# Kernel optimization log

Measured on AMD Instinct MI355X. Metric: run time of the kernel, lower is better.

The kernel has to match this reference:

```python
import jax, jax.numpy as jnp
import numpy as np

DIM, HEADS, HEAD_DIM = 1024, 16, 64
B, L, S = 4, 2048, 2048
EPS = 1e-5
NEG_INF = -1e9


def rms_norm(x, w):
    # x: [..., d]; normalize over last dim, scale by learned weight w [d]
    var = jnp.mean(jnp.square(x), axis=-1, keepdims=True)
    return x * jax.lax.rsqrt(var + EPS) * w


def setup_inputs() -> dict:
    key = jax.random.key(0)
    ks = jax.random.split(key, 9)
    hd = HEADS * HEAD_DIM
    scale = 1.0 / np.sqrt(DIM)
    return {
        "q": jax.random.normal(ks[0], (B, L, DIM), dtype=jnp.float32),
        "kv": jax.random.normal(ks[1], (B, S, DIM), dtype=jnp.float32),
        "x_seqlens": jax.random.randint(ks[2], (B,), 1, S + 1, dtype=jnp.int32),
        "Wq": jax.random.normal(ks[3], (DIM, hd), dtype=jnp.float32) * scale,
        "Wk": jax.random.normal(ks[4], (DIM, hd), dtype=jnp.float32) * scale,
        "Wv": jax.random.normal(ks[5], (DIM, hd), dtype=jnp.float32) * scale,
        "Wo": jax.random.normal(ks[6], (hd, DIM), dtype=jnp.float32) * (1.0 / np.sqrt(hd)),
        "q_norm_w": jnp.ones((HEAD_DIM,), dtype=jnp.float32),
        "k_norm_w": jnp.ones((HEAD_DIM,), dtype=jnp.float32),
    }


def reference(q, kv, x_seqlens, Wq, Wk, Wv, Wo, q_norm_w, k_norm_w):
    b, l, _ = q.shape
    s = kv.shape[1]
    # QKV projections -> [b, h, n, d]
    qh = (q @ Wq).reshape(b, l, HEADS, HEAD_DIM).transpose(0, 2, 1, 3)
    kh = (kv @ Wk).reshape(b, s, HEADS, HEAD_DIM).transpose(0, 2, 1, 3)
    vh = (kv @ Wv).reshape(b, s, HEADS, HEAD_DIM).transpose(0, 2, 1, 3)
    # per-head RMSNorm on q and k
    qh = rms_norm(qh, q_norm_w)
    kh = rms_norm(kh, k_norm_w)
    # dense padding mask [b, 1, 1, s]: True where kv position is valid
    mask = (jnp.arange(s, dtype=jnp.int32)[None, :] < x_seqlens[:, None])[:, None, None, :]
    # scaled dot-product attention (math path: full score matrix)
    scores = jnp.einsum("bhld,bhsd->bhls", qh, kh) * (1.0 / np.sqrt(HEAD_DIM))
    scores = jnp.where(mask, scores, NEG_INF)
    attn = jax.nn.softmax(scores, axis=-1)
    o = jnp.einsum("bhls,bhsd->bhld", attn, vh)  # [b, h, l, d]
    o = o.transpose(0, 2, 1, 3).reshape(b, l, HEADS * HEAD_DIM)
    return o @ Wo
```

## Files before the change

### kernel.cpp

```cpp
#include <hip/hip_runtime.h>
#include <hip/hip_bf16.h>
#include <stdint.h>

#define BB 4
#define LL 2048
#define SS 2048
#define DIMM 1024
#define HH 16
#define HD 64
#define NHD 1024

typedef __bf16 bf16_t;
typedef __bf16 bf16x8 __attribute__((ext_vector_type(8)));
typedef __bf16 bf16x4 __attribute__((ext_vector_type(4)));
typedef float f32x4 __attribute__((ext_vector_type(4)));

#define GLDS16(g, l) __builtin_amdgcn_global_load_lds( \
    (const __attribute__((address_space(1))) void*)(g), \
    (__attribute__((address_space(3))) void*)(l), 16, 0, 0)

#define FENCED_BARRIER() do {                    \
    asm volatile("" ::: "memory");               \
    __builtin_amdgcn_s_barrier();                \
    asm volatile("" ::: "memory");               \
    __builtin_amdgcn_sched_barrier(0);           \
  } while (0)

#define SWZ(o) ((o) ^ ((((o) >> 7) & 7) << 4))

__global__ __launch_bounds__(256) void cvt_all(const float* __restrict__ q,
                                               const float* __restrict__ kv,
                                               bf16_t* __restrict__ Aq,
                                               bf16_t* __restrict__ Akv) {
  const int bi = blockIdx.x;
  const float* in = (bi < 4096) ? q : kv;
  bf16_t* out = (bi < 4096) ? Aq : Akv;
  size_t i = ((size_t)(bi & 4095) * 256 + threadIdx.x) * 8;
  const f32x4* p = (const f32x4*)(in + i);
  f32x4 a = p[0], b = p[1];
  bf16x8 o;
#pragma unroll
  for (int j = 0; j < 4; ++j) { o[j] = (bf16_t)a[j]; o[4 + j] = (bf16_t)b[j]; }
  *(bf16x8*)(out + i) = o;
}

__global__ __launch_bounds__(256) void transpose_all(
    const float* __restrict__ W0, const float* __restrict__ W1,
    const float* __restrict__ W2, const float* __restrict__ W3,
    bf16_t* __restrict__ O0, bf16_t* __restrict__ O1,
    bf16_t* __restrict__ O2, bf16_t* __restrict__ O3) {
  const float* in = (blockIdx.z == 0) ? W0 : (blockIdx.z == 1) ? W1
                    : (blockIdx.z == 2) ? W2 : W3;
  bf16_t* out = (blockIdx.z == 0) ? O0 : (blockIdx.z == 1) ? O1
                : (blockIdx.z == 2) ? O2 : O3;
  __shared__ float tile[64][65];
  const int r0 = blockIdx.y * 64, c0 = blockIdx.x * 64;
  const int tr = threadIdx.x >> 2;
  const int tc4 = (threadIdx.x & 3) * 16;
#pragma unroll
  for (int i = 0; i < 4; ++i) {
    f32x4 v = *(const f32x4*)&in[(size_t)(r0 + tr) * 1024 + c0 + tc4 + i * 4];
    tile[tr][tc4 + i * 4 + 0] = v.x;
    tile[tr][tc4 + i * 4 + 1] = v.y;
    tile[tr][tc4 + i * 4 + 2] = v.z;
    tile[tr][tc4 + i * 4 + 3] = v.w;
  }
  __syncthreads();
#pragma unroll
  for (int i = 0; i < 2; ++i) {
    bf16x8 o;
#pragma unroll
    for (int j = 0; j < 8; ++j) o[j] = (bf16_t)tile[tc4 + i * 8 + j][tr];
    *(bf16x8*)&out[(size_t)(c0 + tr) * 1024 + r0 + tc4 + i * 8] = o;
  }
}

__global__ __launch_bounds__(512, 1) void proj_qkv(
    const bf16_t* __restrict__ Aq, const bf16_t* __restrict__ Akv,
    const bf16_t* __restrict__ WqT, const bf16_t* __restrict__ WkT,
    const bf16_t* __restrict__ WvT,
    bf16_t* __restrict__ Qb, bf16_t* __restrict__ Kb, bf16_t* __restrict__ Vt,
    const float* __restrict__ qw, const float* __restrict__ kw, float qscale) {
  __shared__ bf16_t Lds[2][3][8192];
  const int nt = blockIdx.x;
  const int mode = nt >> 3;
  const bf16_t* A  = (mode == 0) ? Aq : Akv;
  const bf16_t* Bt = (mode == 0) ? WqT : (mode == 1 ? WkT : WvT);
  const int n0 = (nt & 7) * 128;
  const int m0 = blockIdx.y * 256;
  const int tid = threadIdx.x, lane = tid & 63, w = tid >> 6;
  const int wr = w >> 1, wc = w & 1;
  const int fr = lane & 15, fg = lane >> 4;
  f32x4 acc[4][4] = {};

  auto stageKT = [&](int kt, int d) {
#pragma unroll
    for (int ht = 0; ht < 3; ++ht) {
#pragma unroll
      for (int c = 0; c < 2; ++c) {
        const int o = (c * 512 + tid) * 16;
        const int eff = SWZ(o);
        const int rl = eff >> 7, ce = (eff & 127) >> 1;
        const bf16_t* src = (ht < 2)
            ? A  + (size_t)(m0 + ht * 128 + rl) * 1024 + kt * 64 + ce
            : Bt + (size_t)(n0 + rl) * 1024 + kt * 64 + ce;
        GLDS16(src, &Lds[d][ht][c * 4096 + w * 512]);
      }
    }
  };

  stageKT(0, 0);
  int cur = 0;
  for (int kt = 0; kt < 16; ++kt) {
    if (kt + 1 < 16) {
      stageKT(kt + 1, cur ^ 1);
      asm volatile("s_waitcnt vmcnt(6)" ::: "memory");
    } else {
      asm volatile("s_waitcnt vmcnt(0)" ::: "memory");
    }
    FENCED_BARRIER();

    bf16x8 af[4][2], bf[4][2];
#pragma unroll
    for (int m = 0; m < 4; ++m)
#pragma unroll
      for (int ks = 0; ks < 2; ++ks) {
        const int row = wr * 64 + m * 16 + fr;
        const int o = (row & 127) * 128 + ks * 64 + fg * 16;
        af[m][ks] = *(const bf16x8*)&Lds[cur][row >> 7][SWZ(o) >> 1];
      }
#pragma unroll
    for (int n = 0; n < 4; ++n)
#pragma unroll
      for (int ks = 0; ks < 2; ++ks) {
        const int row = wc * 64 + n * 16 + fr;
        const int o = row * 128 + ks * 64 + fg * 16;
        bf[n][ks] = *(const bf16x8*)&Lds[cur][2][SWZ(o) >> 1];
      }
    __builtin_amdgcn_s_setprio(1);
#pragma unroll
    for (int m = 0; m < 4; ++m)
#pragma unroll
      for (int n = 0; n < 4; ++n)
#pragma unroll
        for (int ks = 0; ks < 2; ++ks)
          acc[m][n] = __builtin_amdgcn_mfma_f32_16x16x32_bf16(
              af[m][ks], bf[n][ks], acc[m][n], 0, 0, 0);
    __builtin_amdgcn_s_setprio(0);
    FENCED_BARRIER();
    cur ^= 1;
  }

  if (mode <= 1) {
    const float* nw = (mode == 0) ? qw : kw;
    const float ps = (mode == 0) ? qscale : 1.0f;
    bf16_t* Cb = (mode == 0) ? Qb : Kb;
    float w4[4];
#pragma unroll
    for (int n = 0; n < 4; ++n) w4[n] = nw[n * 16 + fr] * ps;
#pragma unroll
    for (int m = 0; m < 4; ++m) {
      float ss[4];
#pragma unroll
      for (int j = 0; j < 4; ++j) {
        ss[j] = 0.f;
#pragma unroll
        for (int n = 0; n < 4; ++n) ss[j] += acc[m][n][j] * acc[m][n][j];
      }
#pragma unroll
      for (int d = 1; d < 16; d <<= 1)
#pragma unroll
        for (int j = 0; j < 4; ++j) ss[j] += __shfl_xor(ss[j], d);
      float rs[4];
#pragma unroll
      for (int j = 0; j < 4; ++j) rs[j] = rsqrtf(ss[j] * (1.f / 64.f) + 1e-5f);
#pragma unroll
      for (int n = 0; n < 4; ++n)
#pragma unroll
        for (int j = 0; j < 4; ++j) {
          size_t row = (size_t)m0 + wr * 64 + m * 16 + fg * 4 + j;
          size_t col = (size_t)n0 + wc * 64 + n * 16 + fr;
          Cb[row * NHD + col] = (bf16_t)(acc[m][n][j] * rs[j] * w4[n]);
        }
    }
  } else {
#pragma unroll
    for (int m = 0; m < 4; ++m) {
      int r = m0 + wr * 64 + m * 16 + fg * 4;
      int bb_ = r >> 11, s0 = r & 2047;
#pragma unroll
      for (int n = 0; n < 4; ++n) {
        int cc = n0 + wc * 64 + n * 16 + fr;
        int hh_ = cc >> 6, dd = cc & 63;
        bf16x4 pk;
#pragma unroll
        for (int j = 0; j < 4; ++j) pk[j] = (bf16_t)acc[m][n][j];
        *(bf16x4*)&Vt[(((size_t)bb_ * 16 + hh_) * 64 + dd) * 2048 + s0] = pk;
      }
    }
  }
}

__global__ __launch_bounds__(256) void gemm_out(const bf16_t* __restrict__ A,
                                                const bf16_t* __restrict__ Bt,
                                                float* __restrict__ Cout) {
  __shared__ bf16_t As[2][4096];
  __shared__ bf16_t Bs[2][4096];
  const int K = 1024, N = 1024;
  const int tid = threadIdx.x, lane = tid & 63, w = tid >> 6;
  const int m0 = blockIdx.y * 128, n0 = blockIdx.x * 128;
  const int wm = (w >> 1) * 64, wn = (w & 1) * 64;
  const int fr = lane & 15, fg = lane >> 4;
  f32x4 acc[4][4] = {};

  auto stage = [&](int kt, int bi) {
    const int kb = kt * 32;
#pragma unroll
    for (int j = 0; j < 2; ++j) {
      int e = (j * 4 + w) * 512 + lane * 8;
      int r = e >> 5, c = e & 31;
      GLDS16(A  + (size_t)(m0 + r) * K + kb + c, &As[bi][(j * 4 + w) * 512]);
      GLDS16(Bt + (size_t)(n0 + r) * K + kb + c, &Bs[bi][(j * 4 + w) * 512]);
    }
  };

  stage(0, 0);
  int cur = 0;
  for (int kt = 0; kt < 32; ++kt) {
    if (kt + 1 < 32) {
      stage(kt + 1, cur ^ 1);
      asm volatile("s_waitcnt vmcnt(4)" ::: "memory");
    } else {
      asm volatile("s_waitcnt vmcnt(0)" ::: "memory");
    }
    FENCED_BARRIER();
    bf16x8 a[4], b[4];
#pragma unroll
    for (int m = 0; m < 4; ++m) a[m] = *(const bf16x8*)&As[cur][(wm + m * 16 + fr) * 32 + fg * 8];
#pragma unroll
    for (int n = 0; n < 4; ++n) b[n] = *(const bf16x8*)&Bs[cur][(wn + n * 16 + fr) * 32 + fg * 8];
    __builtin_amdgcn_s_setprio(1);
#pragma unroll
    for (int m = 0; m < 4; ++m)
#pragma unroll
      for (int n = 0; n < 4; ++n)
        acc[m][n] = __builtin_amdgcn_mfma_f32_16x16x32_bf16(a[m], b[n], acc[m][n], 0, 0, 0);
    __builtin_amdgcn_s_setprio(0);
    FENCED_BARRIER();
    cur ^= 1;
  }
#pragma unroll
  for (int m = 0; m < 4; ++m)
#pragma unroll
    for (int n = 0; n < 4; ++n)
#pragma unroll
      for (int j = 0; j < 4; ++j) {
        size_t row = (size_t)m0 + wm + m * 16 + fg * 4 + j;
        size_t col = (size_t)n0 + wn + n * 16 + fr;
        Cout[row * N + col] = acc[m][n][j];
      }
}

__global__ __launch_bounds__(256, 3) void attn64(const bf16_t* __restrict__ Qb,
                                                 const bf16_t* __restrict__ Kb,
                                                 const bf16_t* __restrict__ Vtg,
                                                 bf16_t* __restrict__ Ob,
                                                 const int* __restrict__ seqlens) {
  __shared__ bf16_t Kl[2][4096];
  __shared__ bf16_t Vl[2][4096];
  __shared__ bf16_t Pl[8192];
  const int tid = threadIdx.x, lane = tid & 63, w = tid >> 6;
  const int fr = lane & 15, fg = lane >> 4;
  const int qt = blockIdx.x, bh = blockIdx.y;
  const int b = bh >> 4, h = bh & 15;
  const int seqlen = seqlens[b];
  const int ntiles = (seqlen + 63) >> 6;
  bf16_t* Pw = &Pl[w * 2048];

  const bf16_t* qp = Qb + ((size_t)b * LL + qt * 128 + w * 32 + fr) * NHD + h * 64;
  bf16x8 qf[2][2];
#pragma unroll
  for (int qs = 0; qs < 2; ++qs) {
    qf[qs][0] = *(const bf16x8*)&qp[(size_t)qs * 16 * NHD + fg * 8];
    qf[qs][1] = *(const bf16x8*)&qp[(size_t)qs * 16 * NHD + 32 + fg * 8];
  }
  asm volatile("s_waitcnt vmcnt(0)" ::: "memory");

  const bf16_t* Kg = Kb + (size_t)b * SS * NHD + h * 64;
  const bf16_t* Vg = Vtg + ((size_t)(b * 16 + h)) * 64 * SS;

  auto stage = [&](int t, int bi) {
#pragma unroll
    for (int c = 0; c < 2; ++c) {
      const int ro = (w * 2 + c) * 8 + (lane >> 3);
      const int cs = ((lane & 7) ^ (ro & 7)) * 8;
      GLDS16(Kg + (size_t)(t * 64 + ro) * NHD + cs, &Kl[bi][(w * 2 + c) * 512]);
      GLDS16(Vg + (size_t)ro * SS + t * 64 + cs, &Vl[bi][(w * 2 + c) * 512]);
    }
  };

  bf16x8 vones;
#pragma unroll
  for (int i = 0; i < 8; ++i) vones[i] = (bf16_t)1.0f;

  f32x4 oacc[2][4] = {};
  f32x4 lacc[2] = {};
  const float M0 = 12.0f;

  auto softmax_strip = [&](f32x4 (&s)[4], int qs, int t) {
    if (t == ntiles - 1 && (seqlen & 63)) {
#pragma unroll
      for (int n = 0; n < 4; ++n) {
        bool valid = (t * 64 + n * 16 + fr) < seqlen;
#pragma unroll
        for (int j = 0; j < 4; ++j) s[n][j] = valid ? s[n][j] : -1e30f;
      }
    }
#pragma unroll
    for (int n = 0; n < 4; ++n)
#pragma unroll
      for (int j = 0; j < 4; ++j) s[n][j] = __builtin_exp2f(s[n][j] - M0);
#pragma unroll
    for (int n = 0; n < 4; ++n)
#pragma unroll
      for (int j = 0; j < 4; ++j) {
        const int prow = qs * 16 + fg * 4 + j;
        const int pcol = n * 16 + fr;
        Pw[prow * 64 + (((pcol >> 3) ^ (prow & 7)) * 8) + (pcol & 7)] =
            (bf16_t)s[n][j];
      }
  };

  stage(0, 0);
  int cur = 0;
  for (int t = 0; t < ntiles; ++t) {
    if (t + 1 < ntiles) {
      stage(t + 1, cur ^ 1);
      asm volatile("s_waitcnt vmcnt(4)" ::: "memory");
    } else {
      asm volatile("s_waitcnt vmcnt(0)" ::: "memory");
    }
    FENCED_BARRIER();

    f32x4 s0[4] = {}, s1[4] = {};
    __builtin_amdgcn_s_setprio(1);
#pragma unroll
    for (int n = 0; n < 4; ++n) {
      const int rr = n * 16 + fr;
      bf16x8 kf0 = *(const bf16x8*)&Kl[cur][rr * 64 + ((fg ^ (rr & 7)) * 8)];
      bf16x8 kf1 = *(const bf16x8*)&Kl[cur][rr * 64 + (((fg + 4) ^ (rr & 7)) * 8)];
      s0[n] = __builtin_amdgcn_mfma_f32_16x16x32_bf16(qf[0][0], kf0, s0[n], 0, 0, 0);
      s0[n] = __builtin_amdgcn_mfma_f32_16x16x32_bf16(qf[0][1], kf1, s0[n], 0, 0, 0);
      s1[n] = __builtin_amdgcn_mfma_f32_16x16x32_bf16(qf[1][0], kf0, s1[n], 0, 0, 0);
      s1[n] = __builtin_amdgcn_mfma_f32_16x16x32_bf16(qf[1][1], kf1, s1[n], 0, 0, 0);
    }
    __builtin_amdgcn_s_setprio(0);

    softmax_strip(s0, 0, t);
    softmax_strip(s1, 1, t);

    asm volatile("s_waitcnt lgkmcnt(0)" ::: "memory");
    __builtin_amdgcn_sched_barrier(0);

    __builtin_amdgcn_s_setprio(1);
#pragma unroll
    for (int ks = 0; ks < 2; ++ks) {
      const int pr0 = fr, pr1 = 16 + fr;
      bf16x8 pa0 = *(const bf16x8*)&Pw[pr0 * 64 + (((ks * 4 + fg) ^ (pr0 & 7)) * 8)];
      bf16x8 pa1 = *(const bf16x8*)&Pw[pr1 * 64 + (((ks * 4 + fg) ^ (pr1 & 7)) * 8)];
#pragma unroll
      for (int n = 0; n < 4; ++n) {
        const int rr = n * 16 + fr;
        bf16x8 vf = *(const bf16x8*)&Vl[cur][rr * 64 + (((ks * 4 + fg) ^ (rr & 7)) * 8)];
        oacc[0][n] = __builtin_amdgcn_mfma_f32_16x16x32_bf16(pa0, vf, oacc[0][n], 0, 0, 0);
        oacc[1][n] = __builtin_amdgcn_mfma_f32_16x16x32_bf16(pa1, vf, oacc[1][n], 0, 0, 0);
      }
      lacc[0] = __builtin_amdgcn_mfma_f32_16x16x32_bf16(pa0, vones, lacc[0], 0, 0, 0);
      lacc[1] = __builtin_amdgcn_mfma_f32_16x16x32_bf16(pa1, vones, lacc[1], 0, 0, 0);
    }
    __builtin_amdgcn_s_setprio(0);
    FENCED_BARRIER();
    cur ^= 1;
  }

#pragma unroll
  for (int qs = 0; qs < 2; ++qs) {
    float inv[4];
#pragma unroll
    for (int j = 0; j < 4; ++j) inv[j] = __builtin_amdgcn_rcpf(lacc[qs][j]);
#pragma unroll
    for (int n = 0; n < 4; ++n)
#pragma unroll
      for (int j = 0; j < 4; ++j) {
        size_t row = (size_t)b * LL + qt * 128 + w * 32 + qs * 16 + fg * 4 + j;
        Ob[row * NHD + h * 64 + n * 16 + fr] = (bf16_t)(oacc[qs][n][j] * inv[j]);
      }
  }
}

extern "C" void kernel_launch(void* const* d_in, const int* in_sizes, int n_in,
                              void* d_out, int out_size, void* d_ws, size_t ws_size,
                              hipStream_t stream) {
  const float* q   = (const float*)d_in[0];
  const float* kv  = (const float*)d_in[1];
  const int* seqlens = (const int*)d_in[2];
  const float* Wq = (const float*)d_in[3];
  const float* Wk = (const float*)d_in[4];
  const float* Wv = (const float*)d_in[5];
  const float* Wo = (const float*)d_in[6];
  const float* qw = (const float*)d_in[7];
  const float* kw = (const float*)d_in[8];

  char* ws = (char*)d_ws;
  const size_t MB = 1 << 20;
  bf16_t* Aq  = (bf16_t*)(ws + 0 * MB);
  bf16_t* Akv = (bf16_t*)(ws + 16 * MB);
  bf16_t* WqT = (bf16_t*)(ws + 32 * MB);
  bf16_t* WkT = (bf16_t*)(ws + 34 * MB);
  bf16_t* WvT = (bf16_t*)(ws + 36 * MB);
  bf16_t* WoT = (bf16_t*)(ws + 38 * MB);
  bf16_t* Qb  = (bf16_t*)(ws + 40 * MB);
  bf16_t* Kb  = (bf16_t*)(ws + 56 * MB);
  bf16_t* Vt  = (bf16_t*)(ws + 72 * MB);

  const float QSCALE = 0.125f * 1.44269504088896f;

  cvt_all<<<8192, 256, 0, stream>>>(q, kv, Aq, Akv);
  dim3 tg(16, 16, 4);
  transpose_all<<<tg, 256, 0, stream>>>(Wq, Wk, Wv, Wo, WqT, WkT, WvT, WoT);
  dim3 pg(24, 32);
  proj_qkv<<<pg, 512, 0, stream>>>(Aq, Akv, WqT, WkT, WvT, Qb, Kb, Vt,
                                   qw, kw, QSCALE);
  dim3 ag(LL / 128, BB * HH);
  attn64<<<ag, 256, 0, stream>>>(Qb, Kb, Vt, Aq, seqlens);
  dim3 og(8, 64);
  gemm_out<<<og, 256, 0, stream>>>(Aq, WoT, (float*)d_out);
}
```

Baseline: 187.6 us.

## Shrink QKV projection tiles to 128x128 and give output GEMM K=64 swizzled staging

```diff
diff --git a/kernel.cpp b/kernel.cpp
--- a/kernel.cpp
+++ b/kernel.cpp
@@ -75,36 +75,36 @@
   }
 }
 
-__global__ __launch_bounds__(512, 1) void proj_qkv(
+__global__ __launch_bounds__(256, 2) void proj_qkv(
     const bf16_t* __restrict__ Aq, const bf16_t* __restrict__ Akv,
     const bf16_t* __restrict__ WqT, const bf16_t* __restrict__ WkT,
     const bf16_t* __restrict__ WvT,
     bf16_t* __restrict__ Qb, bf16_t* __restrict__ Kb, bf16_t* __restrict__ Vt,
     const float* __restrict__ qw, const float* __restrict__ kw, float qscale) {
-  __shared__ bf16_t Lds[2][3][8192];
+  __shared__ bf16_t Lds[2][2][8192];
   const int nt = blockIdx.x;
   const int mode = nt >> 3;
   const bf16_t* A  = (mode == 0) ? Aq : Akv;
   const bf16_t* Bt = (mode == 0) ? WqT : (mode == 1 ? WkT : WvT);
   const int n0 = (nt & 7) * 128;
-  const int m0 = blockIdx.y * 256;
+  const int m0 = blockIdx.y * 128;
   const int tid = threadIdx.x, lane = tid & 63, w = tid >> 6;
-  const int wr = w >> 1, wc = w & 1;
+  const int wm = (w >> 1) * 64, wn = (w & 1) * 64;
   const int fr = lane & 15, fg = lane >> 4;
   f32x4 acc[4][4] = {};
 
   auto stageKT = [&](int kt, int d) {
 #pragma unroll
-    for (int ht = 0; ht < 3; ++ht) {
-#pragma unroll
-      for (int c = 0; c < 2; ++c) {
-        const int o = (c * 512 + tid) * 16;
+    for (int ht = 0; ht < 2; ++ht) {
+#pragma unroll
+      for (int c = 0; c < 4; ++c) {
+        const int o = (c * 256 + tid) * 16;
         const int eff = SWZ(o);
         const int rl = eff >> 7, ce = (eff & 127) >> 1;
-        const bf16_t* src = (ht < 2)
-            ? A  + (size_t)(m0 + ht * 128 + rl) * 1024 + kt * 64 + ce
+        const bf16_t* src = (ht == 0)
+            ? A  + (size_t)(m0 + rl) * 1024 + kt * 64 + ce
             : Bt + (size_t)(n0 + rl) * 1024 + kt * 64 + ce;
-        GLDS16(src, &Lds[d][ht][c * 4096 + w * 512]);
+        GLDS16(src, &Lds[d][ht][(c * 256 + tid) * 8]);
       }
     }
   };
@@ -114,7 +114,7 @@
   for (int kt = 0; kt < 16; ++kt) {
     if (kt + 1 < 16) {
       stageKT(kt + 1, cur ^ 1);
-      asm volatile("s_waitcnt vmcnt(6)" ::: "memory");
+      asm volatile("s_waitcnt vmcnt(8)" ::: "memory");
     } else {
       asm volatile("s_waitcnt vmcnt(0)" ::: "memory");
     }
@@ -125,17 +125,15 @@
     for (int m = 0; m < 4; ++m)
 #pragma unroll
       for (int ks = 0; ks < 2; ++ks) {
-        const int row = wr * 64 + m * 16 + fr;
-        const int o = (row & 127) * 128 + ks * 64 + fg * 16;
-        af[m][ks] = *(const bf16x8*)&Lds[cur][row >> 7][SWZ(o) >> 1];
+        const int o = (wm + m * 16 + fr) * 128 + ks * 64 + fg * 16;
+        af[m][ks] = *(const bf16x8*)&Lds[cur][0][SWZ(o) >> 1];
       }
 #pragma unroll
     for (int n = 0; n < 4; ++n)
 #pragma unroll
       for (int ks = 0; ks < 2; ++ks) {
-        const int row = wc * 64 + n * 16 + fr;
-        const int o = row * 128 + ks * 64 + fg * 16;
-        bf[n][ks] = *(const bf16x8*)&Lds[cur][2][SWZ(o) >> 1];
+        const int o = (wn + n * 16 + fr) * 128 + ks * 64 + fg * 16;
+        bf[n][ks] = *(const bf16x8*)&Lds[cur][1][SWZ(o) >> 1];
       }
     __builtin_amdgcn_s_setprio(1);
 #pragma unroll
@@ -178,19 +176,19 @@
       for (int n = 0; n < 4; ++n)
 #pragma unroll
         for (int j = 0; j < 4; ++j) {
-          size_t row = (size_t)m0 + wr * 64 + m * 16 + fg * 4 + j;
-          size_t col = (size_t)n0 + wc * 64 + n * 16 + fr;
+          size_t row = (size_t)m0 + wm + m * 16 + fg * 4 + j;
+          size_t col = (size_t)n0 + wn + n * 16 + fr;
           Cb[row * NHD + col] = (bf16_t)(acc[m][n][j] * rs[j] * w4[n]);
         }
     }
   } else {
 #pragma unroll
     for (int m = 0; m < 4; ++m) {
-      int r = m0 + wr * 64 + m * 16 + fg * 4;
+      int r = m0 + wm + m * 16 + fg * 4;
       int bb_ = r >> 11, s0 = r & 2047;
 #pragma unroll
       for (int n = 0; n < 4; ++n) {
-        int cc = n0 + wc * 64 + n * 16 + fr;
+        int cc = n0 + wn + n * 16 + fr;
         int hh_ = cc >> 6, dd = cc & 63;
         bf16x4 pk;
 #pragma unroll
@@ -201,50 +199,67 @@
   }
 }
 
-__global__ __launch_bounds__(256) void gemm_out(const bf16_t* __restrict__ A,
-                                                const bf16_t* __restrict__ Bt,
-                                                float* __restrict__ Cout) {
-  __shared__ bf16_t As[2][4096];
-  __shared__ bf16_t Bs[2][4096];
-  const int K = 1024, N = 1024;
+__global__ __launch_bounds__(256, 2) void gemm_out(const bf16_t* __restrict__ A,
+                                                   const bf16_t* __restrict__ Bt,
+                                                   float* __restrict__ Cout) {
+  __shared__ bf16_t Lds[2][2][8192];
+  const int N = 1024;
   const int tid = threadIdx.x, lane = tid & 63, w = tid >> 6;
   const int m0 = blockIdx.y * 128, n0 = blockIdx.x * 128;
   const int wm = (w >> 1) * 64, wn = (w & 1) * 64;
   const int fr = lane & 15, fg = lane >> 4;
   f32x4 acc[4][4] = {};
 
-  auto stage = [&](int kt, int bi) {
-    const int kb = kt * 32;
-#pragma unroll
-    for (int j = 0; j < 2; ++j) {
-      int e = (j * 4 + w) * 512 + lane * 8;
-      int r = e >> 5, c = e & 31;
-      GLDS16(A  + (size_t)(m0 + r) * K + kb + c, &As[bi][(j * 4 + w) * 512]);
-      GLDS16(Bt + (size_t)(n0 + r) * K + kb + c, &Bs[bi][(j * 4 + w) * 512]);
+  auto stageKT = [&](int kt, int d) {
+#pragma unroll
+    for (int ht = 0; ht < 2; ++ht) {
+#pragma unroll
+      for (int c = 0; c < 4; ++c) {
+        const int o = (c * 256 + tid) * 16;
+        const int eff = SWZ(o);
+        const int rl = eff >> 7, ce = (eff & 127) >> 1;
+        const bf16_t* src = (ht == 0)
+            ? A  + (size_t)(m0 + rl) * 1024 + kt * 64 + ce
+            : Bt + (size_t)(n0 + rl) * 1024 + kt * 64 + ce;
+        GLDS16(src, &Lds[d][ht][(c * 256 + tid) * 8]);
+      }
     }
   };
 
-  stage(0, 0);
+  stageKT(0, 0);
   int cur = 0;
-  for (int kt = 0; kt < 32; ++kt) {
-    if (kt + 1 < 32) {
-      stage(kt + 1, cur ^ 1);
-      asm volatile("s_waitcnt vmcnt(4)" ::: "memory");
+  for (int kt = 0; kt < 16; ++kt) {
+    if (kt + 1 < 16) {
+      stageKT(kt + 1, cur ^ 1);
+      asm volatile("s_waitcnt vmcnt(8)" ::: "memory");
     } else {
       asm volatile("s_waitcnt vmcnt(0)" ::: "memory");
     }
     FENCED_BARRIER();
-    bf16x8 a[4], b[4];
-#pragma unroll
-    for (int m = 0; m < 4; ++m) a[m] = *(const bf16x8*)&As[cur][(wm + m * 16 + fr) * 32 + fg * 8];
-#pragma unroll
-    for (int n = 0; n < 4; ++n) b[n] = *(const bf16x8*)&Bs[cur][(wn + n * 16 + fr) * 32 + fg * 8];
+    bf16x8 af[4][2], bf[4][2];
+#pragma unroll
+    for (int m = 0; m < 4; ++m)
+#pragma unroll
+      for (int ks = 0; ks < 2; ++ks) {
+        const int o = (wm + m * 16 + fr) * 128 + ks * 64 + fg * 16;
+        af[m][ks] = *(const bf16x8*)&Lds[cur][0][SWZ(o) >> 1];
+      }
+#pragma unroll
+    for (int n = 0; n < 4; ++n)
+#pragma unroll
+      for (int ks = 0; ks < 2; ++ks) {
+        const int o = (wn + n * 16 + fr) * 128 + ks * 64 + fg * 16;
+        bf[n][ks] = *(const bf16x8*)&Lds[cur][1][SWZ(o) >> 1];
+      }
     __builtin_amdgcn_s_setprio(1);
 #pragma unroll
     for (int m = 0; m < 4; ++m)
 #pragma unroll
       for (int n = 0; n < 4; ++n)
-        acc[m][n] = __builtin_amdgcn_mfma_f32_16x16x32_bf16(a[m], b[n], acc[m][n], 0, 0, 0);
+#pragma unroll
+        for (int ks = 0; ks < 2; ++ks)
+          acc[m][n] = __builtin_amdgcn_mfma_f32_16x16x32_bf16(
+              af[m][ks], bf[n][ks], acc[m][n], 0, 0, 0);
     __builtin_amdgcn_s_setprio(0);
     FENCED_BARRIER();
     cur ^= 1;
@@ -428,8 +443,8 @@
   cvt_all<<<8192, 256, 0, stream>>>(q, kv, Aq, Akv);
   dim3 tg(16, 16, 4);
   transpose_all<<<tg, 256, 0, stream>>>(Wq, Wk, Wv, Wo, WqT, WkT, WvT, WoT);
-  dim3 pg(24, 32);
-  proj_qkv<<<pg, 512, 0, stream>>>(Aq, Akv, WqT, WkT, WvT, Qb, Kb, Vt,
+  dim3 pg(24, 64);
+  proj_qkv<<<pg, 256, 0, stream>>>(Aq, Akv, WqT, WkT, WvT, Qb, Kb, Vt,
                                    qw, kw, QSCALE);
   dim3 ag(LL / 128, BB * HH);
   attn64<<<ag, 256, 0, stream>>>(Qb, Kb, Vt, Aq, seqlens);
```

Result: no change. 185.7 us (-1.0%).
